# Kernel tuning notes

Measured on AMD Instinct MI355X. Metric: run time of the kernel, lower is better.

## Reference

```python
import jax, jax.numpy as jnp
import numpy as np

# Config constants (match init_kwargs)
E = 16          # n_routed_experts
G = 4           # n_groups
TOPK_G = 2      # topk_groups
K = 4           # n_activated_experts
ROUTE_SCALE = 2.5446


def setup_inputs() -> dict:
    key = jax.random.key(0)
    ks = jax.random.split(key, 9)
    T, D, H = 2048, 1024, 704
    HS = 2 * H  # shared FFN hidden = n_shared_experts * expert_hidden_dim
    sc = lambda k, shape, fan_in: (jax.random.normal(k, shape, jnp.float32)
                                   * (fan_in ** -0.5))
    return {
        "x":      jax.random.normal(ks[0], (T, D), jnp.float32),
        "gate_w": sc(ks[1], (E, D), D),
        "gate_b": jnp.zeros((E,), jnp.float32),       # V3 routing bias (init 0)
        "w1":     sc(ks[2], (E, H, D), D),            # gate proj per expert
        "w3":     sc(ks[3], (E, H, D), D),            # up proj per expert
        "w2":     sc(ks[4], (E, D, H), H),            # down proj per expert
        "ws1":    sc(ks[5], (HS, D), D),              # shared FFN gate proj
        "ws3":    sc(ks[6], (HS, D), D),              # shared FFN up proj
        "ws2":    sc(ks[7], (D, HS), HS),             # shared FFN down proj
    }


def _gate(x, gate_w, gate_b):
    """DeepSeek-V3 sigmoid gate with bias routing + group-limited masking."""
    T = x.shape[0]
    logits = x @ gate_w.T                                   # [T, E]
    scores = jax.nn.sigmoid(logits).astype(jnp.float32)     # original_scores
    routing = scores + gate_b                               # bias only affects routing
    g = routing.reshape(T, G, E // G)
    # use_bias=True -> group score = sum of top-2 routing scores in group
    group_scores = jnp.sum(jax.lax.top_k(g, 2)[0], axis=-1)     # [T, G]
    top_groups = jax.lax.top_k(group_scores, TOPK_G)[1]         # [T, TOPK_G]
    keep = jnp.any(jnp.arange(G)[None, :, None] == top_groups[:, None, :],
                   axis=-1)                                     # [T, G]
    routing = jnp.where(keep[:, :, None], g, -jnp.inf).reshape(T, E)
    idx = jax.lax.top_k(routing, K)[1]                          # [T, K]
    w = jnp.take_along_axis(scores, idx, axis=1)                # un-biased weights
    w = w / jnp.clip(jnp.sum(w, axis=-1, keepdims=True), 1e-9)  # sigmoid renorm
    w = (w * ROUTE_SCALE).astype(x.dtype)
    return w, idx


def reference(x, gate_w, gate_b, w1, w3, w2, ws1, ws3, ws2):
    T, D = x.shape
    weights, idx = _gate(x, gate_w, gate_b)                 # [T,K], [T,K]
    # Dense dispatch/combine matrix: combine[t, e] = gate weight (0 if unrouted)
    combine = jnp.zeros((T, E), x.dtype).at[
        jnp.arange(T)[:, None], idx].add(weights)           # [T, E]
    # Routed experts: SwiGLU per expert, grouped GEMMs
    hg = jnp.einsum('td,ehd->eth', x, w1)                   # [E, T, H]
    hu = jnp.einsum('td,ehd->eth', x, w3)                   # [E, T, H]
    eo = jnp.einsum('eth,edh->etd', jax.nn.silu(hg) * hu, w2)  # [E, T, D]
    y_routed = jnp.einsum('etd,te->td', eo, combine)        # [T, D]
    # Shared experts (always active SwiGLU)
    y_shared = (jax.nn.silu(x @ ws1.T) * (x @ ws3.T)) @ ws2.T
    return y_routed + y_shared
```

## Files before the change

kernel.cpp:

```cpp
#include <hip/hip_runtime.h>
#include <hip/hip_bf16.h>
#include <math.h>

typedef __attribute__((ext_vector_type(4))) float   f32x4;
typedef __attribute__((ext_vector_type(8))) short   short8;
typedef __attribute__((ext_vector_type(8))) __bf16  bf16x8;

union SB8 { short8 s; bf16x8 b; };

__device__ __forceinline__ short f2bf(float f) {
  union { float f; unsigned u; } v; v.f = f;
  unsigned r = v.u + 0x7fffu + ((v.u >> 16) & 1u);
  return (short)(r >> 16);
}

__device__ __forceinline__ short8 cvt8(f32x4 a, f32x4 b) {
  short8 r;
  r[0] = f2bf(a[0]); r[1] = f2bf(a[1]); r[2] = f2bf(a[2]); r[3] = f2bf(a[3]);
  r[4] = f2bf(b[0]); r[5] = f2bf(b[1]); r[6] = f2bf(b[2]); r[7] = f2bf(b[3]);
  return r;
}

__device__ __forceinline__ void ldsload16(const short* g, short* l) {
  __builtin_amdgcn_global_load_lds(
      (const __attribute__((address_space(1))) unsigned int*)g,
      (__attribute__((address_space(3))) unsigned int*)l, 16, 0, 0);
}

#define TT   2048
#define DD   1024
#define HH   704
#define HSS  1408
#define EE   16
#define CAP  2048

#define O1  2097152ULL
#define O2  13631488ULL
#define O3  25165824ULL
#define O4  36700160ULL
#define O5  38141952ULL
#define O6  39583744ULL
#define CVT_TOTAL 41025536ULL
#define CVT_BLOCKS 5008

__global__ __launch_bounds__(256)
void cvt_gate(const float* __restrict__ x,  const float* __restrict__ w1,
              const float* __restrict__ w3, const float* __restrict__ w2,
              const float* __restrict__ s1, const float* __restrict__ s3,
              const float* __restrict__ s2, short* __restrict__ dst,
              const float* __restrict__ gw, const float* __restrict__ gb,
              int* __restrict__ counts, int* __restrict__ tok,
              float* __restrict__ wgt, int* __restrict__ eslot)
{
  if (blockIdx.x < CVT_BLOCKS) {
    const size_t blk = (size_t)blockIdx.x * 8192;
    #pragma unroll
    for (int k = 0; k < 4; k++) {
      size_t i = blk + (size_t)k * 2048 + (size_t)threadIdx.x * 8;
      const float* src;
      if      (i < O1) src = x  + i;
      else if (i < O2) src = w1 + (i - O1);
      else if (i < O3) src = w3 + (i - O2);
      else if (i < O4) src = w2 + (i - O3);
      else if (i < O5) src = s1 + (i - O4);
      else if (i < O6) src = s3 + (i - O5);
      else             src = s2 + (i - O6);
      f32x4 a = *(const f32x4*)src;
      f32x4 b = *(const f32x4*)(src + 4);
      *(short8*)(dst + i) = cvt8(a, b);
    }
    return;
  }

  const int lane = threadIdx.x & 63;
  const int wid  = threadIdx.x >> 6;
  const int t    = (blockIdx.x - CVT_BLOCKS) * 4 + wid;
  const int e    = lane & 15;
  const int p    = lane >> 4;

  const float* xp = x + (size_t)t * DD + p * 256;
  const float* gp = gw + (size_t)e * DD + p * 256;

  double acc = 0.0;
  #pragma unroll 8
  for (int i = 0; i < 64; i++) {
    f32x4 xa = *(const f32x4*)(xp + i * 4);
    f32x4 ga = *(const f32x4*)(gp + i * 4);
    acc += (double)xa[0] * (double)ga[0];
    acc += (double)xa[1] * (double)ga[1];
    acc += (double)xa[2] * (double)ga[2];
    acc += (double)xa[3] * (double)ga[3];
  }
  acc += __shfl_xor(acc, 16);
  acc += __shfl_xor(acc, 32);
  float accf = (float)acc;

  float lf[EE], sc[EE], r[EE];
  #pragma unroll
  for (int j = 0; j < EE; j++) lf[j] = __shfl(accf, j);
  #pragma unroll
  for (int j = 0; j < EE; j++) {
    sc[j] = 1.f / (1.f + expf(-lf[j]));
    r[j] = sc[j] + gb[j];
  }
  float gs[4];
  #pragma unroll
  for (int g = 0; g < 4; g++) {
    float m1 = -1e30f, m2 = -1e30f;
    #pragma unroll
    for (int j = 0; j < 4; j++) {
      float v = r[g * 4 + j];
      if (v > m1) { m2 = m1; m1 = v; }
      else if (v > m2) { m2 = v; }
    }
    gs[g] = m1 + m2;
  }
  int g1 = 0, g2 = -1; float b1 = -1e30f, b2 = -1e30f;
  #pragma unroll
  for (int g = 0; g < 4; g++) {
    if (gs[g] > b1) { b2 = b1; g2 = g1; b1 = gs[g]; g1 = g; }
    else if (gs[g] > b2) { b2 = gs[g]; g2 = g; }
  }
  int idx[4]; float wv[4]; float wsum = 0.f;
  unsigned used = 0;
  #pragma unroll
  for (int k = 0; k < 4; k++) {
    float best = -1e30f; int bi = 0;
    #pragma unroll
    for (int j = 0; j < EE; j++) {
      int g = j >> 2;
      bool keep = (g == g1) || (g == g2);
      if (keep && !((used >> j) & 1) && r[j] > best) { best = r[j]; bi = j; }
    }
    used |= 1u << bi; idx[k] = bi; wv[k] = sc[bi]; wsum += sc[bi];
  }
  float div = wsum < 1e-9f ? 1e-9f : wsum;
  if (lane < 4) {
    float w = wv[lane] / div * 2.5446f;
    int slot = atomicAdd(&counts[idx[lane]], 1);
    tok[idx[lane] * CAP + slot] = t;
    wgt[idx[lane] * CAP + slot] = w;
    eslot[t * 4 + lane] = (idx[lane] << 16) | slot;
  }
}

__global__ __launch_bounds__(256, 2)
void gemm1_merged(const short* __restrict__ xb, const short* __restrict__ w1b,
                  const short* __restrict__ w3b, const short* __restrict__ ws1b,
                  const short* __restrict__ ws3b, short* __restrict__ act_r,
                  short* __restrict__ act_s, const int* __restrict__ counts,
                  const int* __restrict__ tok)
{
  const int z = blockIdx.z;
  const bool routed = (z < EE);
  const int Mt = blockIdx.y, Nt = blockIdx.x;

  int cnt, N, rowbase = 0;
  const short *W1, *W3;
  short* act;
  if (routed) {
    if (Nt >= 6) return;
    cnt = counts[z];
    if (Mt * 128 >= cnt) return;
    int rb = 0;
    for (int i = 0; i < z; i++) rb += counts[i];
    rowbase = rb;
    N = HH;
    W1 = w1b + (size_t)z * HH * DD;
    W3 = w3b + (size_t)z * HH * DD;
    act = act_r;
  } else {
    cnt = TT; N = HSS; W1 = ws1b; W3 = ws3b; act = act_s;
  }

  __shared__ __align__(16) short lA[128 * 64];
  __shared__ __align__(16) short lB1[128 * 64];
  __shared__ __align__(16) short lB3[128 * 64];

  const int tid = threadIdx.x, lane = tid & 63, wv = tid >> 6;
  const int srow = lane >> 3, schunk = lane & 7, scg = schunk ^ srow;

  const short* pa[4]; const short* pb1[4]; const short* pb3[4];
  #pragma unroll
  for (int i = 0; i < 4; i++) {
    const int g = wv * 4 + i;
    int arow = Mt * 128 + g * 8 + srow;
    if (routed) {
      int slot = arow < cnt ? arow : cnt - 1;
      arow = tok[z * CAP + slot];
    }
    pa[i] = xb + (size_t)arow * DD + scg * 8;
    const int brow = Nt * 128 + g * 8 + srow;
    pb1[i] = W1 + (size_t)brow * DD + scg * 8;
    pb3[i] = W3 + (size_t)brow * DD + scg * 8;
  }

  f32x4 acc1[8][2], acc3[8][2];
  #pragma unroll
  for (int i = 0; i < 8; i++) {
    #pragma unroll
    for (int j = 0; j < 2; j++) { acc1[i][j] = (f32x4)0.f; acc3[i][j] = (f32x4)0.f; }
  }

  const int q = lane >> 4, r7 = lane & 7, hi = (lane & 15) >> 3;

  for (int kk = 0; kk < DD; kk += 64) {
    #pragma unroll
    for (int i = 0; i < 4; i++) {
      const int g = wv * 4 + i;
      ldsload16(pa[i] + kk,  lA  + g * 512);
      ldsload16(pb1[i] + kk, lB1 + g * 512);
      ldsload16(pb3[i] + kk, lB3 + g * 512);
    }
    __syncthreads();
    #pragma unroll
    for (int kc = 0; kc < 2; kc++) {
      const int cx = (kc * 4 + q) ^ r7;
      SB8 b1f[2], b3f[2];
      #pragma unroll
      for (int ntl = 0; ntl < 2; ntl++) {
        const int a16 = ((wv * 2 + ntl) * 2 + hi) * 64 + r7 * 8 + cx;
        b1f[ntl].s = *(const short8*)(lB1 + a16 * 8);
        b3f[ntl].s = *(const short8*)(lB3 + a16 * 8);
      }
      #pragma unroll
      for (int mt = 0; mt < 8; mt++) {
        const int a16 = (2 * mt + hi) * 64 + r7 * 8 + cx;
        SB8 af; af.s = *(const short8*)(lA + a16 * 8);
        acc1[mt][0] = __builtin_amdgcn_mfma_f32_16x16x32_bf16(af.b, b1f[0].b, acc1[mt][0], 0, 0, 0);
        acc1[mt][1] = __builtin_amdgcn_mfma_f32_16x16x32_bf16(af.b, b1f[1].b, acc1[mt][1], 0, 0, 0);
        acc3[mt][0] = __builtin_amdgcn_mfma_f32_16x16x32_bf16(af.b, b3f[0].b, acc3[mt][0], 0, 0, 0);
        acc3[mt][1] = __builtin_amdgcn_mfma_f32_16x16x32_bf16(af.b, b3f[1].b, acc3[mt][1], 0, 0, 0);
      }
    }
    __syncthreads();
  }

  const int quad = lane >> 4, lcol = lane & 15;
  #pragma unroll
  for (int mt = 0; mt < 8; mt++) {
    #pragma unroll
    for (int ntl = 0; ntl < 2; ntl++) {
      const int col = Nt * 128 + (wv * 2 + ntl) * 16 + lcol;
      #pragma unroll
      for (int rg = 0; rg < 4; rg++) {
        const int r = Mt * 128 + mt * 16 + quad * 4 + rg;
        if (r < cnt && col < N) {
          float g = acc1[mt][ntl][rg], u = acc3[mt][ntl][rg];
          float a = g / (1.f + __expf(-g)) * u;
          act[(size_t)(rowbase + r) * N + col] = f2bf(a);
        }
      }
    }
  }
}

__global__ __launch_bounds__(256, 2)
void gemm2_merged(const short* __restrict__ act_r, const short* __restrict__ act_s,
                  const short* __restrict__ w2b, const short* __restrict__ ws2b,
                  float* __restrict__ y, float* __restrict__ outr,
                  const int* __restrict__ counts, const float* __restrict__ wgt)
{
  const int z = blockIdx.z;
  const bool routed = (z < EE);
  const int Mt = blockIdx.y, Nt = blockIdx.x;

  int cnt, Kd, rowbase = 0;
  const short *A, *W;
  if (routed) {
    cnt = counts[z];
    if (Mt * 128 >= cnt) return;
    int rb = 0;
    for (int i = 0; i < z; i++) rb += counts[i];
    rowbase = rb;
    Kd = HH;
    A = act_r + (size_t)rowbase * HH;
    W = w2b + (size_t)z * DD * HH;
  } else {
    cnt = TT; Kd = HSS; A = act_s; W = ws2b;
  }

  __shared__ __align__(16) short lA[128 * 64];
  __shared__ __align__(16) short lB[128 * 64];

  const int tid = threadIdx.x, lane = tid & 63, wv = tid >> 6;
  const int srow = lane >> 3, schunk = lane & 7, scg = schunk ^ srow;

  const short* pa[4]; const short* pb[4];
  #pragma unroll
  for (int i = 0; i < 4; i++) {
    const int g = wv * 4 + i;
    int arow = Mt * 128 + g * 8 + srow;
    if (arow >= cnt) arow = cnt - 1;
    pa[i] = A + (size_t)arow * Kd + scg * 8;
    const int brow = Nt * 128 + g * 8 + srow;
    pb[i] = W + (size_t)brow * Kd + scg * 8;
  }

  f32x4 acc[8][2];
  #pragma unroll
  for (int i = 0; i < 8; i++) { acc[i][0] = (f32x4)0.f; acc[i][1] = (f32x4)0.f; }

  const int q = lane >> 4, r7 = lane & 7, hi = (lane & 15) >> 3;

  for (int kk = 0; kk < Kd; kk += 64) {
    #pragma unroll
    for (int i = 0; i < 4; i++) {
      const int g = wv * 4 + i;
      ldsload16(pa[i] + kk, lA + g * 512);
      ldsload16(pb[i] + kk, lB + g * 512);
    }
    __syncthreads();
    #pragma unroll
    for (int kc = 0; kc < 2; kc++) {
      const int cx = (kc * 4 + q) ^ r7;
      SB8 bf[2];
      #pragma unroll
      for (int ntl = 0; ntl < 2; ntl++) {
        const int a16 = ((wv * 2 + ntl) * 2 + hi) * 64 + r7 * 8 + cx;
        bf[ntl].s = *(const short8*)(lB + a16 * 8);
      }
      #pragma unroll
      for (int mt = 0; mt < 8; mt++) {
        const int a16 = (2 * mt + hi) * 64 + r7 * 8 + cx;
        SB8 af; af.s = *(const short8*)(lA + a16 * 8);
        acc[mt][0] = __builtin_amdgcn_mfma_f32_16x16x32_bf16(af.b, bf[0].b, acc[mt][0], 0, 0, 0);
        acc[mt][1] = __builtin_amdgcn_mfma_f32_16x16x32_bf16(af.b, bf[1].b, acc[mt][1], 0, 0, 0);
      }
    }
    __syncthreads();
  }

  const int quad = lane >> 4, lcol = lane & 15;
  #pragma unroll
  for (int mt = 0; mt < 8; mt++) {
    #pragma unroll
    for (int ntl = 0; ntl < 2; ntl++) {
      const int col = Nt * 128 + (wv * 2 + ntl) * 16 + lcol;
      #pragma unroll
      for (int rg = 0; rg < 4; rg++) {
        const int slot = Mt * 128 + mt * 16 + quad * 4 + rg;
        const float v = acc[mt][ntl][rg];
        if (routed) {
          if (slot < cnt) {
            const float w = wgt[z * CAP + slot];
            outr[(size_t)(rowbase + slot) * DD + col] = w * v;
          }
        } else {
          y[(size_t)slot * DD + col] = v;
        }
      }
    }
  }
}

__global__ __launch_bounds__(256)
void combine_kernel(float* __restrict__ y, const float* __restrict__ outr,
                    const int* __restrict__ eslot, const int* __restrict__ counts)
{
  const int t = blockIdx.x;
  const int d = threadIdx.x * 4;

  int offs[EE];
  int s = 0;
  #pragma unroll
  for (int i = 0; i < EE; i++) { offs[i] = s; s += counts[i]; }

  f32x4 accv = *(f32x4*)(y + (size_t)t * DD + d);
  #pragma unroll
  for (int k = 0; k < 4; k++) {
    const int es = eslot[t * 4 + k];
    const int row = offs[es >> 16] + (es & 0xFFFF);
    accv += *(const f32x4*)(outr + (size_t)row * DD + d);
  }
  *(f32x4*)(y + (size_t)t * DD + d) = accv;
}

extern "C" void kernel_launch(void* const* d_in, const int* in_sizes, int n_in,
                              void* d_out, int out_size, void* d_ws, size_t ws_size,
                              hipStream_t stream) {
  const float* x      = (const float*)d_in[0];
  const float* gate_w = (const float*)d_in[1];
  const float* gate_b = (const float*)d_in[2];
  const float* w1     = (const float*)d_in[3];
  const float* w3     = (const float*)d_in[4];
  const float* w2     = (const float*)d_in[5];
  const float* ws1    = (const float*)d_in[6];
  const float* ws3    = (const float*)d_in[7];
  const float* ws2    = (const float*)d_in[8];
  float* y = (float*)d_out;

  char* ws = (char*)d_ws;
  int*   counts = (int*)ws;
  int*   tok    = (int*)(ws + 1024);
  float* wgt    = (float*)(ws + 1024 + (size_t)EE * CAP * 4);
  int*   eslot  = (int*)(ws + 1024 + (size_t)EE * CAP * 8);
  short* bf     = (short*)(ws + 1024 + (size_t)EE * CAP * 8 + (size_t)TT * 16);
  short* xb   = bf;
  short* w1b  = bf + O1;
  short* w3b  = bf + O2;
  short* w2b  = bf + O3;
  short* ws1b = bf + O4;
  short* ws3b = bf + O5;
  short* ws2b = bf + O6;
  short* act_r = bf + CVT_TOTAL;
  short* act_s = act_r + (size_t)8192 * HH;
  float* outr = (float*)(bf + O1);

  (void)hipMemsetAsync(counts, 0, 256, stream);

  cvt_gate<<<CVT_BLOCKS + TT / 4, 256, 0, stream>>>(
      x, w1, w3, w2, ws1, ws3, ws2, bf,
      gate_w, gate_b, counts, tok, wgt, eslot);

  gemm1_merged<<<dim3(11, TT / 128, EE + 1), 256, 0, stream>>>(
      xb, w1b, w3b, ws1b, ws3b, act_r, act_s, counts, tok);

  gemm2_merged<<<dim3(DD / 128, TT / 128, EE + 1), 256, 0, stream>>>(
      act_r, act_s, w2b, ws2b, y, outr, counts, wgt);

  combine_kernel<<<TT, 256, 0, stream>>>(y, outr, eslot, counts);
}
```

Measured before the change: 355.2 us.

## Split gate from conversion, shrink GEMM M tiles, load B fragments directly

Splits the fused convert+gate kernel into a separate gate kernel and a flat conversion kernel that handles 16 elements per thread. The gate dot product now uses four independent double accumulators instead of one serial chain. Both GEMMs drop from 128-row to 64-row M tiles and load B fragments from global memory straight into registers, so only A is staged in LDS. That frees LDS and raises the occupancy hints, in exchange for uncoalesced, unshared B loads that each wave re-reads per M tile, doubling weight traffic.

```diff
diff --git a/kernel.cpp b/kernel.cpp
--- a/kernel.cpp
+++ b/kernel.cpp
@@ -41,56 +41,57 @@
 #define O5  38141952ULL
 #define O6  39583744ULL
 #define CVT_TOTAL 41025536ULL
-#define CVT_BLOCKS 5008
+#define CVT_BLOCKS 10016
 
 __global__ __launch_bounds__(256)
-void cvt_gate(const float* __restrict__ x,  const float* __restrict__ w1,
-              const float* __restrict__ w3, const float* __restrict__ w2,
-              const float* __restrict__ s1, const float* __restrict__ s3,
-              const float* __restrict__ s2, short* __restrict__ dst,
-              const float* __restrict__ gw, const float* __restrict__ gb,
-              int* __restrict__ counts, int* __restrict__ tok,
-              float* __restrict__ wgt, int* __restrict__ eslot)
+void cvt_all(const float* __restrict__ x,  const float* __restrict__ w1,
+             const float* __restrict__ w3, const float* __restrict__ w2,
+             const float* __restrict__ s1, const float* __restrict__ s3,
+             const float* __restrict__ s2, short* __restrict__ dst)
 {
-  if (blockIdx.x < CVT_BLOCKS) {
-    const size_t blk = (size_t)blockIdx.x * 8192;
-    #pragma unroll
-    for (int k = 0; k < 4; k++) {
-      size_t i = blk + (size_t)k * 2048 + (size_t)threadIdx.x * 8;
-      const float* src;
-      if      (i < O1) src = x  + i;
-      else if (i < O2) src = w1 + (i - O1);
-      else if (i < O3) src = w3 + (i - O2);
-      else if (i < O4) src = w2 + (i - O3);
-      else if (i < O5) src = s1 + (i - O4);
-      else if (i < O6) src = s3 + (i - O5);
-      else             src = s2 + (i - O6);
-      f32x4 a = *(const f32x4*)src;
-      f32x4 b = *(const f32x4*)(src + 4);
-      *(short8*)(dst + i) = cvt8(a, b);
-    }
-    return;
-  }
-
+  size_t i = ((size_t)blockIdx.x * 256 + threadIdx.x) * 16;
+  const float* src;
+  if      (i < O1) src = x  + i;
+  else if (i < O2) src = w1 + (i - O1);
+  else if (i < O3) src = w3 + (i - O2);
+  else if (i < O4) src = w2 + (i - O3);
+  else if (i < O5) src = s1 + (i - O4);
+  else if (i < O6) src = s3 + (i - O5);
+  else             src = s2 + (i - O6);
+  f32x4 a0 = *(const f32x4*)(src);
+  f32x4 a1 = *(const f32x4*)(src + 4);
+  f32x4 a2 = *(const f32x4*)(src + 8);
+  f32x4 a3 = *(const f32x4*)(src + 12);
+  *(short8*)(dst + i)     = cvt8(a0, a1);
+  *(short8*)(dst + i + 8) = cvt8(a2, a3);
+}
+
+__global__ __launch_bounds__(256)
+void gate_kernel(const float* __restrict__ x, const float* __restrict__ gw,
+                 const float* __restrict__ gb,
+                 int* __restrict__ counts, int* __restrict__ tok,
+                 float* __restrict__ wgt, int* __restrict__ eslot)
+{
   const int lane = threadIdx.x & 63;
   const int wid  = threadIdx.x >> 6;
-  const int t    = (blockIdx.x - CVT_BLOCKS) * 4 + wid;
+  const int t    = blockIdx.x * 4 + wid;
   const int e    = lane & 15;
   const int p    = lane >> 4;
 
   const float* xp = x + (size_t)t * DD + p * 256;
   const float* gp = gw + (size_t)e * DD + p * 256;
 
-  double acc = 0.0;
+  double a0 = 0.0, a1 = 0.0, a2 = 0.0, a3 = 0.0;
   #pragma unroll 8
   for (int i = 0; i < 64; i++) {
     f32x4 xa = *(const f32x4*)(xp + i * 4);
     f32x4 ga = *(const f32x4*)(gp + i * 4);
-    acc += (double)xa[0] * (double)ga[0];
-    acc += (double)xa[1] * (double)ga[1];
-    acc += (double)xa[2] * (double)ga[2];
-    acc += (double)xa[3] * (double)ga[3];
-  }
+    a0 += (double)xa[0] * (double)ga[0];
+    a1 += (double)xa[1] * (double)ga[1];
+    a2 += (double)xa[2] * (double)ga[2];
+    a3 += (double)xa[3] * (double)ga[3];
+  }
+  double acc = (a0 + a1) + (a2 + a3);
   acc += __shfl_xor(acc, 16);
   acc += __shfl_xor(acc, 32);
   float accf = (float)acc;
@@ -144,7 +145,7 @@
   }
 }
 
-__global__ __launch_bounds__(256, 2)
+__global__ __launch_bounds__(256, 3)
 void gemm1_merged(const short* __restrict__ xb, const short* __restrict__ w1b,
                   const short* __restrict__ w3b, const short* __restrict__ ws1b,
                   const short* __restrict__ ws3b, short* __restrict__ act_r,
@@ -161,7 +162,7 @@
   if (routed) {
     if (Nt >= 6) return;
     cnt = counts[z];
-    if (Mt * 128 >= cnt) return;
+    if (Mt * 64 >= cnt) return;
     int rb = 0;
     for (int i = 0; i < z; i++) rb += counts[i];
     rowbase = rb;
@@ -173,64 +174,63 @@
     cnt = TT; N = HSS; W1 = ws1b; W3 = ws3b; act = act_s;
   }
 
-  __shared__ __align__(16) short lA[128 * 64];
-  __shared__ __align__(16) short lB1[128 * 64];
-  __shared__ __align__(16) short lB3[128 * 64];
+  __shared__ __align__(16) short lA[64 * 64];
 
   const int tid = threadIdx.x, lane = tid & 63, wv = tid >> 6;
-  const int srow = lane >> 3, schunk = lane & 7, scg = schunk ^ srow;
-
-  const short* pa[4]; const short* pb1[4]; const short* pb3[4];
-  #pragma unroll
-  for (int i = 0; i < 4; i++) {
-    const int g = wv * 4 + i;
-    int arow = Mt * 128 + g * 8 + srow;
+  const int srow = lane >> 3, scg = (lane & 7) ^ srow;
+
+  const short* pa[2];
+  #pragma unroll
+  for (int i = 0; i < 2; i++) {
+    const int g = wv * 2 + i;
+    int arow = Mt * 64 + g * 8 + srow;
     if (routed) {
       int slot = arow < cnt ? arow : cnt - 1;
       arow = tok[z * CAP + slot];
     }
     pa[i] = xb + (size_t)arow * DD + scg * 8;
-    const int brow = Nt * 128 + g * 8 + srow;
-    pb1[i] = W1 + (size_t)brow * DD + scg * 8;
-    pb3[i] = W3 + (size_t)brow * DD + scg * 8;
-  }
-
-  f32x4 acc1[8][2], acc3[8][2];
-  #pragma unroll
-  for (int i = 0; i < 8; i++) {
+  }
+
+  const int q = lane >> 4, r7 = lane & 7, hi = (lane & 15) >> 3;
+  const short* pb1[2]; const short* pb3[2];
+  #pragma unroll
+  for (int ntl = 0; ntl < 2; ntl++) {
+    const int brow = Nt * 128 + (wv * 2 + ntl) * 16 + (lane & 15);
+    pb1[ntl] = W1 + (size_t)brow * DD + q * 8;
+    pb3[ntl] = W3 + (size_t)brow * DD + q * 8;
+  }
+
+  f32x4 acc1[4][2], acc3[4][2];
+  #pragma unroll
+  for (int i = 0; i < 4; i++) {
     #pragma unroll
     for (int j = 0; j < 2; j++) { acc1[i][j] = (f32x4)0.f; acc3[i][j] = (f32x4)0.f; }
   }
 
-  const int q = lane >> 4, r7 = lane & 7, hi = (lane & 15) >> 3;
-
   for (int kk = 0; kk < DD; kk += 64) {
     #pragma unroll
-    for (int i = 0; i < 4; i++) {
-      const int g = wv * 4 + i;
-      ldsload16(pa[i] + kk,  lA  + g * 512);
-      ldsload16(pb1[i] + kk, lB1 + g * 512);
-      ldsload16(pb3[i] + kk, lB3 + g * 512);
+    for (int i = 0; i < 2; i++)
+      ldsload16(pa[i] + kk, lA + (wv * 2 + i) * 512);
+    SB8 b1f[2][2], b3f[2][2];
+    #pragma unroll
+    for (int ntl = 0; ntl < 2; ntl++) {
+      b1f[0][ntl].s = *(const short8*)(pb1[ntl] + kk);
+      b3f[0][ntl].s = *(const short8*)(pb3[ntl] + kk);
+      b1f[1][ntl].s = *(const short8*)(pb1[ntl] + kk + 32);
+      b3f[1][ntl].s = *(const short8*)(pb3[ntl] + kk + 32);
     }
     __syncthreads();
     #pragma unroll
     for (int kc = 0; kc < 2; kc++) {
       const int cx = (kc * 4 + q) ^ r7;
-      SB8 b1f[2], b3f[2];
       #pragma unroll
-      for (int ntl = 0; ntl < 2; ntl++) {
-        const int a16 = ((wv * 2 + ntl) * 2 + hi) * 64 + r7 * 8 + cx;
-        b1f[ntl].s = *(const short8*)(lB1 + a16 * 8);
-        b3f[ntl].s = *(const short8*)(lB3 + a16 * 8);
-      }
-      #pragma unroll
-      for (int mt = 0; mt < 8; mt++) {
+      for (int mt = 0; mt < 4; mt++) {
         const int a16 = (2 * mt + hi) * 64 + r7 * 8 + cx;
         SB8 af; af.s = *(const short8*)(lA + a16 * 8);
-        acc1[mt][0] = __builtin_amdgcn_mfma_f32_16x16x32_bf16(af.b, b1f[0].b, acc1[mt][0], 0, 0, 0);
-        acc1[mt][1] = __builtin_amdgcn_mfma_f32_16x16x32_bf16(af.b, b1f[1].b, acc1[mt][1], 0, 0, 0);
-        acc3[mt][0] = __builtin_amdgcn_mfma_f32_16x16x32_bf16(af.b, b3f[0].b, acc3[mt][0], 0, 0, 0);
-        acc3[mt][1] = __builtin_amdgcn_mfma_f32_16x16x32_bf16(af.b, b3f[1].b, acc3[mt][1], 0, 0, 0);
+        acc1[mt][0] = __builtin_amdgcn_mfma_f32_16x16x32_bf16(af.b, b1f[kc][0].b, acc1[mt][0], 0, 0, 0);
+        acc1[mt][1] = __builtin_amdgcn_mfma_f32_16x16x32_bf16(af.b, b1f[kc][1].b, acc1[mt][1], 0, 0, 0);
+        acc3[mt][0] = __builtin_amdgcn_mfma_f32_16x16x32_bf16(af.b, b3f[kc][0].b, acc3[mt][0], 0, 0, 0);
+        acc3[mt][1] = __builtin_amdgcn_mfma_f32_16x16x32_bf16(af.b, b3f[kc][1].b, acc3[mt][1], 0, 0, 0);
       }
     }
     __syncthreads();
@@ -238,13 +238,13 @@
 
   const int quad = lane >> 4, lcol = lane & 15;
   #pragma unroll
-  for (int mt = 0; mt < 8; mt++) {
+  for (int mt = 0; mt < 4; mt++) {
     #pragma unroll
     for (int ntl = 0; ntl < 2; ntl++) {
       const int col = Nt * 128 + (wv * 2 + ntl) * 16 + lcol;
       #pragma unroll
       for (int rg = 0; rg < 4; rg++) {
-        const int r = Mt * 128 + mt * 16 + quad * 4 + rg;
+        const int r = Mt * 64 + mt * 16 + quad * 4 + rg;
         if (r < cnt && col < N) {
           float g = acc1[mt][ntl][rg], u = acc3[mt][ntl][rg];
           float a = g / (1.f + __expf(-g)) * u;
@@ -255,7 +255,7 @@
   }
 }
 
-__global__ __launch_bounds__(256, 2)
+__global__ __launch_bounds__(256, 4)
 void gemm2_merged(const short* __restrict__ act_r, const short* __restrict__ act_s,
                   const short* __restrict__ w2b, const short* __restrict__ ws2b,
                   float* __restrict__ y, float* __restrict__ outr,
@@ -269,7 +269,7 @@
   const short *A, *W;
   if (routed) {
     cnt = counts[z];
-    if (Mt * 128 >= cnt) return;
+    if (Mt * 64 >= cnt) return;
     int rb = 0;
     for (int i = 0; i < z; i++) rb += counts[i];
     rowbase = rb;
@@ -280,52 +280,52 @@
     cnt = TT; Kd = HSS; A = act_s; W = ws2b;
   }
 
-  __shared__ __align__(16) short lA[128 * 64];
-  __shared__ __align__(16) short lB[128 * 64];
+  __shared__ __align__(16) short lA[64 * 64];
 
   const int tid = threadIdx.x, lane = tid & 63, wv = tid >> 6;
-  const int srow = lane >> 3, schunk = lane & 7, scg = schunk ^ srow;
-
-  const short* pa[4]; const short* pb[4];
-  #pragma unroll
-  for (int i = 0; i < 4; i++) {
-    const int g = wv * 4 + i;
-    int arow = Mt * 128 + g * 8 + srow;
+  const int srow = lane >> 3, scg = (lane & 7) ^ srow;
+
+  const short* pa[2];
+  #pragma unroll
+  for (int i = 0; i < 2; i++) {
+    const int g = wv * 2 + i;
+    int arow = Mt * 64 + g * 8 + srow;
     if (arow >= cnt) arow = cnt - 1;
     pa[i] = A + (size_t)arow * Kd + scg * 8;
-    const int brow = Nt * 128 + g * 8 + srow;
-    pb[i] = W + (size_t)brow * Kd + scg * 8;
-  }
-
-  f32x4 acc[8][2];
-  #pragma unroll
-  for (int i = 0; i < 8; i++) { acc[i][0] = (f32x4)0.f; acc[i][1] = (f32x4)0.f; }
+  }
 
   const int q = lane >> 4, r7 = lane & 7, hi = (lane & 15) >> 3;
+  const short* pb[2];
+  #pragma unroll
+  for (int ntl = 0; ntl < 2; ntl++) {
+    const int brow = Nt * 128 + (wv * 2 + ntl) * 16 + (lane & 15);
+    pb[ntl] = W + (size_t)brow * Kd + q * 8;
+  }
+
+  f32x4 acc[4][2];
+  #pragma unroll
+  for (int i = 0; i < 4; i++) { acc[i][0] = (f32x4)0.f; acc[i][1] = (f32x4)0.f; }
 
   for (int kk = 0; kk < Kd; kk += 64) {
     #pragma unroll
-    for (int i = 0; i < 4; i++) {
-      const int g = wv * 4 + i;
-      ldsload16(pa[i] + kk, lA + g * 512);
-      ldsload16(pb[i] + kk, lB + g * 512);
+    for (int i = 0; i < 2; i++)
+      ldsload16(pa[i] + kk, lA + (wv * 2 + i) * 512);
+    SB8 bf[2][2];
+    #pragma unroll
+    for (int ntl = 0; ntl < 2; ntl++) {
+      bf[0][ntl].s = *(const short8*)(pb[ntl] + kk);
+      bf[1][ntl].s = *(const short8*)(pb[ntl] + kk + 32);
     }
     __syncthreads();
     #pragma unroll
     for (int kc = 0; kc < 2; kc++) {
       const int cx = (kc * 4 + q) ^ r7;
-      SB8 bf[2];
       #pragma unroll
-      for (int ntl = 0; ntl < 2; ntl++) {
-        const int a16 = ((wv * 2 + ntl) * 2 + hi) * 64 + r7 * 8 + cx;
-        bf[ntl].s = *(const short8*)(lB + a16 * 8);
-      }
-      #pragma unroll
-      for (int mt = 0; mt < 8; mt++) {
+      for (int mt = 0; mt < 4; mt++) {
         const int a16 = (2 * mt + hi) * 64 + r7 * 8 + cx;
         SB8 af; af.s = *(const short8*)(lA + a16 * 8);
-        acc[mt][0] = __builtin_amdgcn_mfma_f32_16x16x32_bf16(af.b, bf[0].b, acc[mt][0], 0, 0, 0);
-        acc[mt][1] = __builtin_amdgcn_mfma_f32_16x16x32_bf16(af.b, bf[1].b, acc[mt][1], 0, 0, 0);
+        acc[mt][0] = __builtin_amdgcn_mfma_f32_16x16x32_bf16(af.b, bf[kc][0].b, acc[mt][0], 0, 0, 0);
+        acc[mt][1] = __builtin_amdgcn_mfma_f32_16x16x32_bf16(af.b, bf[kc][1].b, acc[mt][1], 0, 0, 0);
       }
     }
     __syncthreads();
@@ -333,13 +333,13 @@
 
   const int quad = lane >> 4, lcol = lane & 15;
   #pragma unroll
-  for (int mt = 0; mt < 8; mt++) {
+  for (int mt = 0; mt < 4; mt++) {
     #pragma unroll
     for (int ntl = 0; ntl < 2; ntl++) {
       const int col = Nt * 128 + (wv * 2 + ntl) * 16 + lcol;
       #pragma unroll
       for (int rg = 0; rg < 4; rg++) {
-        const int slot = Mt * 128 + mt * 16 + quad * 4 + rg;
+        const int slot = Mt * 64 + mt * 16 + quad * 4 + rg;
         const float v = acc[mt][ntl][rg];
         if (routed) {
           if (slot < cnt) {
@@ -409,14 +409,14 @@
 
   (void)hipMemsetAsync(counts, 0, 256, stream);
 
-  cvt_gate<<<CVT_BLOCKS + TT / 4, 256, 0, stream>>>(
-      x, w1, w3, w2, ws1, ws3, ws2, bf,
-      gate_w, gate_b, counts, tok, wgt, eslot);
-
-  gemm1_merged<<<dim3(11, TT / 128, EE + 1), 256, 0, stream>>>(
+  gate_kernel<<<TT / 4, 256, 0, stream>>>(x, gate_w, gate_b, counts, tok, wgt, eslot);
+
+  cvt_all<<<CVT_BLOCKS, 256, 0, stream>>>(x, w1, w3, w2, ws1, ws3, ws2, bf);
+
+  gemm1_merged<<<dim3(11, TT / 64, EE + 1), 256, 0, stream>>>(
       xb, w1b, w3b, ws1b, ws3b, act_r, act_s, counts, tok);
 
-  gemm2_merged<<<dim3(DD / 128, TT / 128, EE + 1), 256, 0, stream>>>(
+  gemm2_merged<<<dim3(DD / 128, TT / 64, EE + 1), 256, 0, stream>>>(
       act_r, act_s, w2b, ws2b, y, outr, counts, wgt);
 
   combine_kernel<<<TT, 256, 0, stream>>>(y, outr, eslot, counts);
```

Measured after the change: 436.9 us. 1.23x slower.
